# Kernel optimization log

Measured on AMD Instinct MI355X. Metric: run time of the kernel, lower is better.

## Reference

```python
import jax, jax.numpy as jnp
import numpy as np

TIME_UNITS = 10.0
EPS_LN = 1e-5
N_NODES, N_EDGES, BATCH, T_IN = 20000, 320000, 8, 12
H_PROB, H_VEL = 64, 32


def _layernorm(x, g, b):
    mu = jnp.mean(x, axis=-1, keepdims=True)
    var = jnp.mean((x - mu) ** 2, axis=-1, keepdims=True)
    return (x - mu) / jnp.sqrt(var + EPS_LN) * g + b


def setup_inputs() -> dict:
    key = jax.random.key(0)
    ks = jax.random.split(key, 20)
    s = 0.1
    inp = {}
    inp['upstream'] = jax.random.uniform(ks[0], (N_EDGES, BATCH, T_IN), jnp.float32)
    inp['downstream'] = jax.random.uniform(ks[1], (N_EDGES, BATCH, T_IN), jnp.float32)
    inp['feature'] = jax.random.uniform(ks[2], (N_NODES, BATCH, T_IN), jnp.float32)
    inp['distance'] = jax.random.uniform(ks[3], (N_EDGES,), jnp.float32, 10.0, 500.0)
    inp['src'] = jax.random.randint(ks[4], (N_EDGES,), 0, N_NODES, jnp.int32)
    inp['dst'] = jax.random.randint(ks[5], (N_EDGES,), 0, N_NODES, jnp.int32)
    inp['fc_w'] = jax.random.normal(ks[6], (H_PROB, T_IN), jnp.float32) * s
    inp['attn_w'] = jax.random.normal(ks[7], (1, 2 * H_PROB + 1), jnp.float32) * s
    inp['ln2_g'] = jnp.ones((2 * H_PROB + 1,), jnp.float32)
    inp['ln2_b'] = jnp.zeros((2 * H_PROB + 1,), jnp.float32)
    inp['v11_w'] = jax.random.normal(ks[8], (H_VEL, T_IN), jnp.float32) * s
    inp['v11_b'] = jnp.zeros((H_VEL,), jnp.float32)
    inp['ln11_g'] = jnp.ones((H_VEL,), jnp.float32)
    inp['ln11_b'] = jnp.zeros((H_VEL,), jnp.float32)
    inp['v12_w'] = jax.random.normal(ks[9], (1, H_VEL), jnp.float32) * s
    inp['v12_b'] = jnp.zeros((1,), jnp.float32)
    inp['v21_w'] = jax.random.normal(ks[10], (H_VEL, T_IN), jnp.float32) * s
    inp['v21_b'] = jnp.zeros((H_VEL,), jnp.float32)
    inp['ln21_g'] = jnp.ones((H_VEL,), jnp.float32)
    inp['ln21_b'] = jnp.zeros((H_VEL,), jnp.float32)
    inp['v22_w'] = jax.random.normal(ks[11], (1, H_VEL), jnp.float32) * s
    inp['v22_b'] = jnp.zeros((1,), jnp.float32)
    inp['v3_w'] = jax.random.normal(ks[12], (1, 2), jnp.float32) * s
    inp['v3_b'] = jnp.zeros((1,), jnp.float32)
    inp['alpha'] = jnp.ones((N_EDGES, 1), jnp.float32)
    return inp


def reference(upstream, downstream, feature, distance, src, dst,
              fc_w, attn_w, ln2_g, ln2_b,
              v11_w, v11_b, ln11_g, ln11_b, v12_w, v12_b,
              v21_w, v21_b, ln21_g, ln21_b, v22_w, v22_b,
              v3_w, v3_b, alpha):
    N, B, T = feature.shape
    Tf = jnp.asarray(T, feature.dtype)

    # --- Velocity_Model_NAM (eval mode: dropout = identity) ---
    def branch(x, w1, b1, g, bn, w2, b2):
        h = jax.nn.relu(_layernorm(x @ w1.T + b1, g, bn))
        return jax.nn.sigmoid(h @ w2.T + b2)  # [E,B,1]

    xu = branch(upstream, v11_w, v11_b, ln11_g, ln11_b, v12_w, v12_b)
    xd = branch(downstream, v21_w, v21_b, ln21_g, ln21_b, v22_w, v22_b)
    v = jnp.log1p(jnp.exp((jnp.concatenate([xu, xd], -1) @ v3_w.T + v3_b)[..., 0]))  # [E,B]

    # --- per-edge travel time and diffusion kernel ---
    Tt = distance[:, None] / (v + 1e-5)                # [E,B]
    T_idx = jnp.round(Tt / TIME_UNITS)
    T_idx = jnp.where(T_idx < 0, 0.0, T_idx)
    T_idx = jnp.where(T_idx > Tf, Tf - 1.0, T_idx)     # strictly > T_in, as in masked_fill
    F = 1.0 / (1.0 + alpha * Tt)                       # [E,B]
    n = jnp.maximum(Tf - T_idx, 1.0)                   # sequence length per (edge,batch)
    t = jnp.arange(T, dtype=feature.dtype)
    mask = t < n[..., None]
    expo = jnp.maximum(n[..., None] - 1.0 - t, 0.0)    # decreasing exponents n-1..0
    diffusion = jnp.where(mask, F[..., None] * jnp.power(1.0 - F[..., None], expo), 0.0)  # [E,B,T]

    # --- Probabilistic_Model: embeddings + edge softmax normalized per SOURCE node ---
    z = feature @ fc_w.T                               # [N,B,64]
    zc = jnp.concatenate([z[src], z[dst], jax.lax.stop_gradient(v)[..., None]], -1)  # [E,B,129]
    a = jax.nn.leaky_relu((_layernorm(zc, ln2_g, ln2_b) @ attn_w.T)[..., 0], 0.01)   # [E,B]
    m = jax.ops.segment_max(a, src, num_segments=N)
    ex = jnp.exp(a - m[src])
    den = jax.ops.segment_sum(ex, src, num_segments=N)
    score = ex / den[src]

    # --- mailbox reduce: attention-weighted diffusion prediction per destination ---
    pred_edge = jnp.sum(diffusion * feature[src], -1)  # [E,B]
    pred = jax.ops.segment_sum(score * pred_edge, dst, num_segments=N)  # [N,B]
    return pred
```

## Files before the change

kernel.cpp:

```cpp
#include <hip/hip_runtime.h>
#include <math.h>

#define TB 8
#define TT 12
#define HV 32

__device__ __forceinline__ float vel_branch32(const float x[TT],
    const float* __restrict__ w1, const float* __restrict__ b1,
    const float* __restrict__ g,  const float* __restrict__ bn,
    const float* __restrict__ w2, float b2) {
  float h[HV];
  float s1 = 0.f, s2 = 0.f;
#pragma unroll
  for (int j = 0; j < HV; ++j) {
    float hj = b1[j];
#pragma unroll
    for (int t = 0; t < TT; ++t) hj = fmaf(x[t], w1[j*TT + t], hj);
    h[j] = hj;
    s1 += hj;
    s2 = fmaf(hj, hj, s2);
  }
  float mu  = s1 * (1.f/HV);
  float var = s2 * (1.f/HV) - mu*mu;
  float inv = 1.f / sqrtf(var + 1e-5f);
  float acc = b2;
#pragma unroll
  for (int j = 0; j < HV; ++j) {
    float yl = fmaf((h[j]-mu)*inv, g[j], bn[j]);
    yl = fmaxf(yl, 0.f);
    acc = fmaf(yl, w2[j], acc);
  }
  return 1.f / (1.f + __expf(-acc));
}

__device__ __noinline__ double vel_branch64(const float* x,
    const float* __restrict__ w1, const float* __restrict__ b1,
    const float* __restrict__ g,  const float* __restrict__ bn,
    const float* __restrict__ w2, float b2) {
  double s1 = 0.0, s2 = 0.0;
  for (int j = 0; j < HV; ++j) {
    double hj = (double)b1[j];
    for (int t = 0; t < TT; ++t) hj = fma((double)x[t], (double)w1[j*TT+t], hj);
    s1 += hj;
    s2 = fma(hj, hj, s2);
  }
  double mu  = s1 / (double)HV;
  double var = s2 / (double)HV - mu*mu;
  double inv = 1.0 / sqrt(var + 1e-5);
  double acc = (double)b2;
  for (int j = 0; j < HV; ++j) {
    double hj = (double)b1[j];
    for (int t = 0; t < TT; ++t) hj = fma((double)x[t], (double)w1[j*TT+t], hj);
    double yl = (hj - mu) * inv * (double)g[j] + (double)bn[j];
    if (yl < 0.0) yl = 0.0;
    acc = fma(yl, (double)w2[j], acc);
  }
  return 1.0 / (1.0 + exp(-acc));
}

__global__ void __launch_bounds__(256) k_zero_prep(
    float* __restrict__ den, float* __restrict__ pred, int nb,
    const float* __restrict__ attn_w, const float* __restrict__ ln2_g,
    const float* __restrict__ ln2_b, float* __restrict__ scal) {
  int idx = blockIdx.x * blockDim.x + threadIdx.x;
  for (int i = idx; i < nb; i += gridDim.x * blockDim.x) { den[i] = 0.f; pred[i] = 0.f; }
  if (blockIdx.x == 0) {
    __shared__ float sg[256], sb[256];
    float a = 0.f, b = 0.f;
    if (threadIdx.x < 129) {
      float w = attn_w[threadIdx.x];
      a = w * ln2_g[threadIdx.x];
      b = w * ln2_b[threadIdx.x];
    }
    sg[threadIdx.x] = a; sb[threadIdx.x] = b;
    __syncthreads();
    for (int s = 128; s > 0; s >>= 1) {
      if (threadIdx.x < s) { sg[threadIdx.x] += sg[threadIdx.x+s]; sb[threadIdx.x] += sb[threadIdx.x+s]; }
      __syncthreads();
    }
    if (threadIdx.x == 0) { scal[0] = sg[0]; scal[1] = sb[0]; }
  }
}

__global__ void __launch_bounds__(256, 2) k_node(
    const float* __restrict__ feature, const float* __restrict__ fc_w,
    const float* __restrict__ attn_w,  const float* __restrict__ ln2_g,
    float4* __restrict__ nodepre, int n_nodes) {
  int idx = blockIdx.x * blockDim.x + threadIdx.x;
  int total = n_nodes * TB;
  if (idx >= total) return;
  const float4* f4 = (const float4*)(feature + (size_t)idx * TT);
  float4 fa = f4[0], fb = f4[1], fcv = f4[2];
  float x[TT] = {fa.x,fa.y,fa.z,fa.w, fb.x,fb.y,fb.z,fb.w, fcv.x,fcv.y,fcv.z,fcv.w};
  float q = 0.f, r = 0.f, ps = 0.f, pd = 0.f;
#pragma unroll 8
  for (int i = 0; i < 64; ++i) {
    float z = 0.f;
#pragma unroll
    for (int t = 0; t < TT; ++t) z = fmaf(x[t], fc_w[i*TT + t], z);
    q += z;
    r  = fmaf(z, z, r);
    ps = fmaf(z, attn_w[i]      * ln2_g[i],      ps);
    pd = fmaf(z, attn_w[64 + i] * ln2_g[64 + i], pd);
  }
  nodepre[idx] = make_float4(q, r, ps, pd);
}

__global__ void __launch_bounds__(256, 2) k_edge1(
    const float* __restrict__ upstream, const float* __restrict__ downstream,
    const float* __restrict__ feature,  const float* __restrict__ distance,
    const int* __restrict__ src, const int* __restrict__ dst,
    const float* __restrict__ attn_w, const float* __restrict__ ln2_g,
    const float* __restrict__ v11_w, const float* __restrict__ v11_b,
    const float* __restrict__ ln11_g, const float* __restrict__ ln11_b,
    const float* __restrict__ v12_w, const float* __restrict__ v12_b,
    const float* __restrict__ v21_w, const float* __restrict__ v21_b,
    const float* __restrict__ ln21_g, const float* __restrict__ ln21_b,
    const float* __restrict__ v22_w, const float* __restrict__ v22_b,
    const float* __restrict__ v3_w, const float* __restrict__ v3_b,
    const float* __restrict__ alpha,
    const float4* __restrict__ nodepre, const float* __restrict__ scal,
    float2* __restrict__ epbuf, float* __restrict__ den,
    int n_edges) {
  int idx = blockIdx.x * blockDim.x + threadIdx.x;
  if (idx >= n_edges * TB) return;
  int e = idx >> 3, b = idx & 7;

  int s = src[e], d = dst[e];
  float dist = distance[e];
  float al   = alpha[e];
  const float4* f4 = (const float4*)(feature + ((size_t)s * TB + b) * TT);
  float4 f0 = f4[0], f1 = f4[1], f2 = f4[2];
  float4 nps = nodepre[(size_t)s * TB + b];
  float4 npd = nodepre[(size_t)d * TB + b];

  float xu, xd;
  {
    const float4* u4 = (const float4*)(upstream + (size_t)idx * TT);
    float4 a0 = u4[0], a1 = u4[1], a2 = u4[2];
    float xin[TT] = {a0.x,a0.y,a0.z,a0.w, a1.x,a1.y,a1.z,a1.w, a2.x,a2.y,a2.z,a2.w};
    xu = vel_branch32(xin, v11_w, v11_b, ln11_g, ln11_b, v12_w, v12_b[0]);
  }
  {
    const float4* d4 = (const float4*)(downstream + (size_t)idx * TT);
    float4 c0 = d4[0], c1 = d4[1], c2 = d4[2];
    float xin[TT] = {c0.x,c0.y,c0.z,c0.w, c1.x,c1.y,c1.z,c1.w, c2.x,c2.y,c2.z,c2.w};
    xd = vel_branch32(xin, v21_w, v21_b, ln21_g, ln21_b, v22_w, v22_b[0]);
  }
  float y  = fmaf(xu, v3_w[0], fmaf(xd, v3_w[1], v3_b[0]));
  float v  = log1pf(expf(y));

  float tt   = dist / (v + 1e-5f);
  float th   = tt * 0.1f;
  float tif  = rintf(th);

  if (fabsf(th - tif) < 1e-3f && tt < 120.0f) {
    const float4* u4 = (const float4*)(upstream + (size_t)idx * TT);
    float4 a0 = u4[0], a1 = u4[1], a2 = u4[2];
    float xiu[TT] = {a0.x,a0.y,a0.z,a0.w, a1.x,a1.y,a1.z,a1.w, a2.x,a2.y,a2.z,a2.w};
    const float4* d4 = (const float4*)(downstream + (size_t)idx * TT);
    float4 c0 = d4[0], c1 = d4[1], c2 = d4[2];
    float xid[TT] = {c0.x,c0.y,c0.z,c0.w, c1.x,c1.y,c1.z,c1.w, c2.x,c2.y,c2.z,c2.w};
    double xu64 = vel_branch64(xiu, v11_w, v11_b, ln11_g, ln11_b, v12_w, v12_b[0]);
    double xd64 = vel_branch64(xid, v21_w, v21_b, ln21_g, ln21_b, v22_w, v22_b[0]);
    double y64  = xu64*(double)v3_w[0] + xd64*(double)v3_w[1] + (double)v3_b[0];
    double v64  = log1p(exp(y64));
    double tt64 = (double)dist / (v64 + 1e-5);
    v   = (float)v64;
    tt  = (float)tt64;
    tif = (float)rint(tt64 * 0.1);
  }

  int ti = (int)tif;
  ti = ti < 0 ? 0 : (ti > TT ? TT - 1 : ti);
  int n = TT - ti; n = n < 1 ? 1 : n;

  float F  = 1.f / fmaf(al, tt, 1.f);
  float om = 1.f - F;

  float feat[TT] = {f0.x,f0.y,f0.z,f0.w, f1.x,f1.y,f1.z,f1.w, f2.x,f2.y,f2.z,f2.w};
  float pe = 0.f, w = F;
#pragma unroll
  for (int t = TT - 1; t >= 0; --t) {
    if (t < n) { pe = fmaf(w, feat[t], pe); w *= om; }
  }

  float sum   = nps.x + npd.x + v;
  float sumsq = nps.y + npd.y + v*v;
  float mu  = sum * (1.f/129.f);
  float var = sumsq * (1.f/129.f) - mu*mu;
  float S1  = nps.z + npd.w + v * attn_w[128] * ln2_g[128];
  float aa  = (S1 - mu*scal[0]) / sqrtf(var + 1e-5f) + scal[1];
  float a   = aa >= 0.f ? aa : 0.01f*aa;
  float ex  = __expf(a);

  epbuf[idx] = make_float2(ex, pe);
  atomicAdd(&den[s * TB + b], ex);
}

__global__ void __launch_bounds__(256) k_edge2(
    const int* __restrict__ src, const int* __restrict__ dst,
    const float2* __restrict__ epbuf,
    const float* __restrict__ den, float* __restrict__ pred, int n_edges) {
  int idx = blockIdx.x * blockDim.x + threadIdx.x;
  if (idx >= n_edges * TB) return;
  int e = idx >> 3, b = idx & 7;
  float2 ep = epbuf[idx];
  float score = ep.x / den[src[e] * TB + b];
  atomicAdd(&pred[dst[e] * TB + b], score * ep.y);
}

extern "C" void kernel_launch(void* const* d_in, const int* in_sizes, int n_in,
                              void* d_out, int out_size, void* d_ws, size_t ws_size,
                              hipStream_t stream) {
  const float* upstream   = (const float*)d_in[0];
  const float* downstream = (const float*)d_in[1];
  const float* feature    = (const float*)d_in[2];
  const float* distance   = (const float*)d_in[3];
  const int*   src        = (const int*)d_in[4];
  const int*   dst        = (const int*)d_in[5];
  const float* fc_w   = (const float*)d_in[6];
  const float* attn_w = (const float*)d_in[7];
  const float* ln2_g  = (const float*)d_in[8];
  const float* ln2_b  = (const float*)d_in[9];
  const float* v11_w  = (const float*)d_in[10];
  const float* v11_b  = (const float*)d_in[11];
  const float* ln11_g = (const float*)d_in[12];
  const float* ln11_b = (const float*)d_in[13];
  const float* v12_w  = (const float*)d_in[14];
  const float* v12_b  = (const float*)d_in[15];
  const float* v21_w  = (const float*)d_in[16];
  const float* v21_b  = (const float*)d_in[17];
  const float* ln21_g = (const float*)d_in[18];
  const float* ln21_b = (const float*)d_in[19];
  const float* v22_w  = (const float*)d_in[20];
  const float* v22_b  = (const float*)d_in[21];
  const float* v3_w   = (const float*)d_in[22];
  const float* v3_b   = (const float*)d_in[23];
  const float* alpha  = (const float*)d_in[24];

  int E  = in_sizes[4];
  int N  = in_sizes[2] / (TB * TT);
  int NB = N * TB;
  int EB = E * TB;

  float*  ws      = (float*)d_ws;
  float4* nodepre = (float4*)ws;
  float2* epbuf   = (float2*)(ws + 4 * (size_t)NB);
  float*  den     = ws + 4 * (size_t)NB + 2 * (size_t)EB;
  float*  scal    = den + NB;
  float*  pred    = (float*)d_out;

  int blk = 256;
  k_zero_prep<<<(NB + blk - 1) / blk, blk, 0, stream>>>(den, pred, NB, attn_w, ln2_g, ln2_b, scal);
  k_node<<<(NB + blk - 1) / blk, blk, 0, stream>>>(feature, fc_w, attn_w, ln2_g, nodepre, N);
  k_edge1<<<(EB + blk - 1) / blk, blk, 0, stream>>>(
      upstream, downstream, feature, distance, src, dst,
      attn_w, ln2_g,
      v11_w, v11_b, ln11_g, ln11_b, v12_w, v12_b,
      v21_w, v21_b, ln21_g, ln21_b, v22_w, v22_b,
      v3_w, v3_b, alpha,
      nodepre, scal, epbuf, den, E);
  k_edge2<<<(EB + blk - 1) / blk, blk, 0, stream>>>(src, dst, epbuf, den, pred, E);
}
```

Before: 196.8 us.

## Process two batch rows per thread with packed v2f FMAs in edge kernels

Each thread in the edge kernels now handles two consecutive batch rows, so index, distance and weight loads are shared and the velocity MLP weights are reused across both rows. Dot products use two-wide float vector FMAs (eligible for packed FP32 math), and the node kernel gets the same treatment. Occupancy hint rises to 3 blocks per SM and epbuf is written as float4. This raises register pressure and halves thread count, which may reduce latency hiding.

```diff
diff --git a/kernel.cpp b/kernel.cpp
--- a/kernel.cpp
+++ b/kernel.cpp
@@ -5,32 +5,51 @@
 #define TT 12
 #define HV 32
 
-__device__ __forceinline__ float vel_branch32(const float x[TT],
+typedef float v2f __attribute__((ext_vector_type(2)));
+
+__device__ __forceinline__ void vel2_rows(
+    const v2f xa[6], const v2f xb[6],
     const float* __restrict__ w1, const float* __restrict__ b1,
     const float* __restrict__ g,  const float* __restrict__ bn,
-    const float* __restrict__ w2, float b2) {
-  float h[HV];
-  float s1 = 0.f, s2 = 0.f;
+    const float* __restrict__ w2, float b2,
+    float& oa, float& ob) {
+  float ha[HV], hb[HV];
+  float s1a = 0.f, s2a = 0.f, s1b = 0.f, s2b = 0.f;
 #pragma unroll
   for (int j = 0; j < HV; ++j) {
-    float hj = b1[j];
-#pragma unroll
-    for (int t = 0; t < TT; ++t) hj = fmaf(x[t], w1[j*TT + t], hj);
-    h[j] = hj;
-    s1 += hj;
-    s2 = fmaf(hj, hj, s2);
-  }
-  float mu  = s1 * (1.f/HV);
-  float var = s2 * (1.f/HV) - mu*mu;
-  float inv = 1.f / sqrtf(var + 1e-5f);
-  float acc = b2;
+    const float* w = w1 + j * TT;
+    v2f pa = {0.f, 0.f}, pb = {0.f, 0.f};
+#pragma unroll
+    for (int k = 0; k < 6; ++k) {
+      v2f wv = *(const v2f*)(w + 2 * k);
+      pa = __builtin_elementwise_fma(xa[k], wv, pa);
+      pb = __builtin_elementwise_fma(xb[k], wv, pb);
+    }
+    float bj  = b1[j];
+    float hja = pa.x + pa.y + bj;
+    float hjb = pb.x + pb.y + bj;
+    ha[j] = hja; hb[j] = hjb;
+    s1a += hja; s2a = fmaf(hja, hja, s2a);
+    s1b += hjb; s2b = fmaf(hjb, hjb, s2b);
+  }
+  float mua  = s1a * (1.f/HV);
+  float vara = s2a * (1.f/HV) - mua*mua;
+  float inva = 1.f / sqrtf(vara + 1e-5f);
+  float mub  = s1b * (1.f/HV);
+  float varb = s2b * (1.f/HV) - mub*mub;
+  float invb = 1.f / sqrtf(varb + 1e-5f);
+  float aa = b2, ab = b2;
 #pragma unroll
   for (int j = 0; j < HV; ++j) {
-    float yl = fmaf((h[j]-mu)*inv, g[j], bn[j]);
-    yl = fmaxf(yl, 0.f);
-    acc = fmaf(yl, w2[j], acc);
-  }
-  return 1.f / (1.f + __expf(-acc));
+    float gj = g[j], bnj = bn[j], w2j = w2[j];
+    float ya = fmaf((ha[j]-mua)*inva, gj, bnj);
+    float yb = fmaf((hb[j]-mub)*invb, gj, bnj);
+    ya = fmaxf(ya, 0.f); yb = fmaxf(yb, 0.f);
+    aa = fmaf(ya, w2j, aa);
+    ab = fmaf(yb, w2j, ab);
+  }
+  oa = 1.f / (1.f + __expf(-aa));
+  ob = 1.f / (1.f + __expf(-ab));
 }
 
 __device__ __noinline__ double vel_branch64(const float* x,
@@ -91,13 +110,15 @@
   if (idx >= total) return;
   const float4* f4 = (const float4*)(feature + (size_t)idx * TT);
   float4 fa = f4[0], fb = f4[1], fcv = f4[2];
-  float x[TT] = {fa.x,fa.y,fa.z,fa.w, fb.x,fb.y,fb.z,fb.w, fcv.x,fcv.y,fcv.z,fcv.w};
+  v2f xv[6] = {{fa.x,fa.y},{fa.z,fa.w},{fb.x,fb.y},{fb.z,fb.w},{fcv.x,fcv.y},{fcv.z,fcv.w}};
   float q = 0.f, r = 0.f, ps = 0.f, pd = 0.f;
 #pragma unroll 8
   for (int i = 0; i < 64; ++i) {
-    float z = 0.f;
-#pragma unroll
-    for (int t = 0; t < TT; ++t) z = fmaf(x[t], fc_w[i*TT + t], z);
+    v2f p = {0.f, 0.f};
+#pragma unroll
+    for (int k = 0; k < 6; ++k)
+      p = __builtin_elementwise_fma(xv[k], *(const v2f*)(fc_w + i*TT + 2*k), p);
+    float z = p.x + p.y;
     q += z;
     r  = fmaf(z, z, r);
     ps = fmaf(z, attn_w[i]      * ln2_g[i],      ps);
@@ -106,7 +127,7 @@
   nodepre[idx] = make_float4(q, r, ps, pd);
 }
 
-__global__ void __launch_bounds__(256, 2) k_edge1(
+__global__ void __launch_bounds__(256, 3) k_edge1(
     const float* __restrict__ upstream, const float* __restrict__ downstream,
     const float* __restrict__ feature,  const float* __restrict__ distance,
     const int* __restrict__ src, const int* __restrict__ dst,
@@ -121,93 +142,115 @@
     const float* __restrict__ alpha,
     const float4* __restrict__ nodepre, const float* __restrict__ scal,
     float2* __restrict__ epbuf, float* __restrict__ den,
-    int n_edges) {
+    int n_pairs) {
   int idx = blockIdx.x * blockDim.x + threadIdx.x;
-  if (idx >= n_edges * TB) return;
-  int e = idx >> 3, b = idx & 7;
+  if (idx >= n_pairs) return;
+  int e    = idx >> 2;
+  int row0 = idx * 2;
+  int b0   = row0 & 7;
 
   int s = src[e], d = dst[e];
   float dist = distance[e];
   float al   = alpha[e];
-  const float4* f4 = (const float4*)(feature + ((size_t)s * TB + b) * TT);
-  float4 f0 = f4[0], f1 = f4[1], f2 = f4[2];
-  float4 nps = nodepre[(size_t)s * TB + b];
-  float4 npd = nodepre[(size_t)d * TB + b];
-
-  float xu, xd;
+  const float4* f4 = (const float4*)(feature + ((size_t)s * TB + b0) * TT);
+  float4 F0 = f4[0], F1 = f4[1], F2 = f4[2], F3 = f4[3], F4 = f4[4], F5 = f4[5];
+  float4 nps0 = nodepre[(size_t)s * TB + b0];
+  float4 nps1 = nodepre[(size_t)s * TB + b0 + 1];
+  float4 npd0 = nodepre[(size_t)d * TB + b0];
+  float4 npd1 = nodepre[(size_t)d * TB + b0 + 1];
+
+  float xu0, xu1, xd0, xd1;
   {
-    const float4* u4 = (const float4*)(upstream + (size_t)idx * TT);
-    float4 a0 = u4[0], a1 = u4[1], a2 = u4[2];
-    float xin[TT] = {a0.x,a0.y,a0.z,a0.w, a1.x,a1.y,a1.z,a1.w, a2.x,a2.y,a2.z,a2.w};
-    xu = vel_branch32(xin, v11_w, v11_b, ln11_g, ln11_b, v12_w, v12_b[0]);
+    const float4* u4 = (const float4*)(upstream + (size_t)row0 * TT);
+    float4 U0=u4[0],U1=u4[1],U2=u4[2],U3=u4[3],U4=u4[4],U5=u4[5];
+    v2f xa[6] = {{U0.x,U0.y},{U0.z,U0.w},{U1.x,U1.y},{U1.z,U1.w},{U2.x,U2.y},{U2.z,U2.w}};
+    v2f xb[6] = {{U3.x,U3.y},{U3.z,U3.w},{U4.x,U4.y},{U4.z,U4.w},{U5.x,U5.y},{U5.z,U5.w}};
+    vel2_rows(xa, xb, v11_w, v11_b, ln11_g, ln11_b, v12_w, v12_b[0], xu0, xu1);
   }
   {
-    const float4* d4 = (const float4*)(downstream + (size_t)idx * TT);
-    float4 c0 = d4[0], c1 = d4[1], c2 = d4[2];
-    float xin[TT] = {c0.x,c0.y,c0.z,c0.w, c1.x,c1.y,c1.z,c1.w, c2.x,c2.y,c2.z,c2.w};
-    xd = vel_branch32(xin, v21_w, v21_b, ln21_g, ln21_b, v22_w, v22_b[0]);
-  }
-  float y  = fmaf(xu, v3_w[0], fmaf(xd, v3_w[1], v3_b[0]));
-  float v  = log1pf(expf(y));
-
-  float tt   = dist / (v + 1e-5f);
-  float th   = tt * 0.1f;
-  float tif  = rintf(th);
-
-  if (fabsf(th - tif) < 1e-3f && tt < 120.0f) {
-    const float4* u4 = (const float4*)(upstream + (size_t)idx * TT);
-    float4 a0 = u4[0], a1 = u4[1], a2 = u4[2];
-    float xiu[TT] = {a0.x,a0.y,a0.z,a0.w, a1.x,a1.y,a1.z,a1.w, a2.x,a2.y,a2.z,a2.w};
-    const float4* d4 = (const float4*)(downstream + (size_t)idx * TT);
-    float4 c0 = d4[0], c1 = d4[1], c2 = d4[2];
-    float xid[TT] = {c0.x,c0.y,c0.z,c0.w, c1.x,c1.y,c1.z,c1.w, c2.x,c2.y,c2.z,c2.w};
-    double xu64 = vel_branch64(xiu, v11_w, v11_b, ln11_g, ln11_b, v12_w, v12_b[0]);
-    double xd64 = vel_branch64(xid, v21_w, v21_b, ln21_g, ln21_b, v22_w, v22_b[0]);
-    double y64  = xu64*(double)v3_w[0] + xd64*(double)v3_w[1] + (double)v3_b[0];
-    double v64  = log1p(exp(y64));
-    double tt64 = (double)dist / (v64 + 1e-5);
-    v   = (float)v64;
-    tt  = (float)tt64;
-    tif = (float)rint(tt64 * 0.1);
-  }
-
-  int ti = (int)tif;
-  ti = ti < 0 ? 0 : (ti > TT ? TT - 1 : ti);
-  int n = TT - ti; n = n < 1 ? 1 : n;
-
-  float F  = 1.f / fmaf(al, tt, 1.f);
-  float om = 1.f - F;
-
-  float feat[TT] = {f0.x,f0.y,f0.z,f0.w, f1.x,f1.y,f1.z,f1.w, f2.x,f2.y,f2.z,f2.w};
-  float pe = 0.f, w = F;
-#pragma unroll
-  for (int t = TT - 1; t >= 0; --t) {
-    if (t < n) { pe = fmaf(w, feat[t], pe); w *= om; }
-  }
-
-  float sum   = nps.x + npd.x + v;
-  float sumsq = nps.y + npd.y + v*v;
-  float mu  = sum * (1.f/129.f);
-  float var = sumsq * (1.f/129.f) - mu*mu;
-  float S1  = nps.z + npd.w + v * attn_w[128] * ln2_g[128];
-  float aa  = (S1 - mu*scal[0]) / sqrtf(var + 1e-5f) + scal[1];
-  float a   = aa >= 0.f ? aa : 0.01f*aa;
-  float ex  = __expf(a);
-
-  epbuf[idx] = make_float2(ex, pe);
-  atomicAdd(&den[s * TB + b], ex);
+    const float4* d4 = (const float4*)(downstream + (size_t)row0 * TT);
+    float4 D0=d4[0],D1=d4[1],D2=d4[2],D3=d4[3],D4=d4[4],D5=d4[5];
+    v2f xa[6] = {{D0.x,D0.y},{D0.z,D0.w},{D1.x,D1.y},{D1.z,D1.w},{D2.x,D2.y},{D2.z,D2.w}};
+    v2f xb[6] = {{D3.x,D3.y},{D3.z,D3.w},{D4.x,D4.y},{D4.z,D4.w},{D5.x,D5.y},{D5.z,D5.w}};
+    vel2_rows(xa, xb, v21_w, v21_b, ln21_g, ln21_b, v22_w, v22_b[0], xd0, xd1);
+  }
+
+  float feat0[TT] = {F0.x,F0.y,F0.z,F0.w, F1.x,F1.y,F1.z,F1.w, F2.x,F2.y,F2.z,F2.w};
+  float feat1[TT] = {F3.x,F3.y,F3.z,F3.w, F4.x,F4.y,F4.z,F4.w, F5.x,F5.y,F5.z,F5.w};
+  float ex_r[2], pe_r[2];
+
+#pragma unroll
+  for (int r = 0; r < 2; ++r) {
+    float xu = r ? xu1 : xu0;
+    float xd = r ? xd1 : xd0;
+    float y  = fmaf(xu, v3_w[0], fmaf(xd, v3_w[1], v3_b[0]));
+    float v  = log1pf(expf(y));
+
+    float tt  = dist / (v + 1e-5f);
+    float th  = tt * 0.1f;
+    float tif = rintf(th);
+
+    if (fabsf(th - tif) < 1e-3f && tt < 120.0f) {
+      const float* xr_u = upstream   + (size_t)(row0 + r) * TT;
+      const float* xr_d = downstream + (size_t)(row0 + r) * TT;
+      double xu64 = vel_branch64(xr_u, v11_w, v11_b, ln11_g, ln11_b, v12_w, v12_b[0]);
+      double xd64 = vel_branch64(xr_d, v21_w, v21_b, ln21_g, ln21_b, v22_w, v22_b[0]);
+      double y64  = xu64*(double)v3_w[0] + xd64*(double)v3_w[1] + (double)v3_b[0];
+      double v64  = log1p(exp(y64));
+      double tt64 = (double)dist / (v64 + 1e-5);
+      v   = (float)v64;
+      tt  = (float)tt64;
+      tif = (float)rint(tt64 * 0.1);
+    }
+
+    int ti = (int)tif;
+    ti = ti < 0 ? 0 : (ti > TT ? TT - 1 : ti);
+    int n = TT - ti; n = n < 1 ? 1 : n;
+
+    float F  = 1.f / fmaf(al, tt, 1.f);
+    float om = 1.f - F;
+
+    const float* feat = r ? feat1 : feat0;
+    float pe = 0.f, w = F;
+#pragma unroll
+    for (int t = TT - 1; t >= 0; --t) {
+      if (t < n) { pe = fmaf(w, feat[t], pe); w *= om; }
+    }
+
+    float4 nps = r ? nps1 : nps0;
+    float4 npd = r ? npd1 : npd0;
+    float sum   = nps.x + npd.x + v;
+    float sumsq = nps.y + npd.y + v*v;
+    float mu  = sum * (1.f/129.f);
+    float var = sumsq * (1.f/129.f) - mu*mu;
+    float S1  = nps.z + npd.w + v * attn_w[128] * ln2_g[128];
+    float aa  = (S1 - mu*scal[0]) / sqrtf(var + 1e-5f) + scal[1];
+    float a   = aa >= 0.f ? aa : 0.01f*aa;
+    ex_r[r] = __expf(a);
+    pe_r[r] = pe;
+  }
+
+  float4 ep4 = make_float4(ex_r[0], pe_r[0], ex_r[1], pe_r[1]);
+  *(float4*)(&epbuf[row0]) = ep4;
+  atomicAdd(&den[s * TB + b0],     ex_r[0]);
+  atomicAdd(&den[s * TB + b0 + 1], ex_r[1]);
 }
 
 __global__ void __launch_bounds__(256) k_edge2(
     const int* __restrict__ src, const int* __restrict__ dst,
     const float2* __restrict__ epbuf,
-    const float* __restrict__ den, float* __restrict__ pred, int n_edges) {
+    const float* __restrict__ den, float* __restrict__ pred, int n_pairs) {
   int idx = blockIdx.x * blockDim.x + threadIdx.x;
-  if (idx >= n_edges * TB) return;
-  int e = idx >> 3, b = idx & 7;
-  float2 ep = epbuf[idx];
-  float score = ep.x / den[src[e] * TB + b];
-  atomicAdd(&pred[dst[e] * TB + b], score * ep.y);
+  if (idx >= n_pairs) return;
+  int e    = idx >> 2;
+  int row0 = idx * 2;
+  int b0   = row0 & 7;
+  float4 ep = *(const float4*)(&epbuf[row0]);
+  int s = src[e], d = dst[e];
+  float den0 = den[s * TB + b0];
+  float den1 = den[s * TB + b0 + 1];
+  atomicAdd(&pred[d * TB + b0],     (ep.x / den0) * ep.y);
+  atomicAdd(&pred[d * TB + b0 + 1], (ep.z / den1) * ep.w);
 }
 
 extern "C" void kernel_launch(void* const* d_in, const int* in_sizes, int n_in,
@@ -243,6 +286,7 @@
   int N  = in_sizes[2] / (TB * TT);
   int NB = N * TB;
   int EB = E * TB;
+  int NP = EB / 2;
 
   float*  ws      = (float*)d_ws;
   float4* nodepre = (float4*)ws;
@@ -254,12 +298,12 @@
   int blk = 256;
   k_zero_prep<<<(NB + blk - 1) / blk, blk, 0, stream>>>(den, pred, NB, attn_w, ln2_g, ln2_b, scal);
   k_node<<<(NB + blk - 1) / blk, blk, 0, stream>>>(feature, fc_w, attn_w, ln2_g, nodepre, N);
-  k_edge1<<<(EB + blk - 1) / blk, blk, 0, stream>>>(
+  k_edge1<<<(NP + blk - 1) / blk, blk, 0, stream>>>(
       upstream, downstream, feature, distance, src, dst,
       attn_w, ln2_g,
       v11_w, v11_b, ln11_g, ln11_b, v12_w, v12_b,
       v21_w, v21_b, ln21_g, ln21_b, v22_w, v22_b,
       v3_w, v3_b, alpha,
-      nodepre, scal, epbuf, den, E);
-  k_edge2<<<(EB + blk - 1) / blk, blk, 0, stream>>>(src, dst, epbuf, den, pred, E);
-}
+      nodepre, scal, epbuf, den, NP);
+  k_edge2<<<(NP + blk - 1) / blk, blk, 0, stream>>>(src, dst, epbuf, den, pred, NP);
+}
```

Result: slower. 352.7 us (+79.2%).
